# Performance work log

Measured on AMD Instinct MI355X. Metric: run time of the kernel, lower is better.

## Reference

```python
import jax, jax.numpy as jnp
import numpy as np

B, IN, H = 131072, 128, 128


def setup_inputs() -> dict:
    key = jax.random.key(0)
    ks = jax.random.split(key, 8)
    scale_W = 1.0 / np.sqrt(IN + H)
    scale_r = 1.0 / np.sqrt(H)
    return {
        "x": jax.random.normal(ks[0], (B, IN), jnp.float32),
        "h": jax.random.normal(ks[1], (B, H), jnp.float32),
        "c": jax.random.normal(ks[2], (B, H), jnp.float32),
        "n": jax.random.uniform(ks[3], (B, H), jnp.float32, 0.1, 1.0),
        "m": jax.random.normal(ks[4], (B, H), jnp.float32),
        "W": jax.random.normal(ks[5], (IN + H, 4 * H), jnp.float32) * scale_W,
        "r": jax.random.normal(ks[6], (H, 4 * H), jnp.float32) * scale_r,
        "b": jnp.zeros((4 * H,), jnp.float32),
    }


def reference(x, h, c, n, m, W, r, b):
    # fused gate pre-activations: [B, 4H]
    combined = jnp.concatenate((x, h), axis=1)
    gates = combined @ W + h @ r + b
    i_raw, f_raw, z_raw, o_raw = jnp.split(gates, 4, axis=1)
    i = jnp.exp(i_raw)
    f = jax.nn.sigmoid(f_raw)
    z = jnp.tanh(z_raw)
    o = jax.nn.sigmoid(o_raw)
    # log-domain stabilizer (max trick), faithful to source incl. m overwrite
    m_new = jnp.maximum(jnp.log(f) + m, jnp.log(i))
    i_prime = jnp.exp(jnp.log(i) - m_new)
    f_prime = jnp.exp(jnp.log(f) + m_new - m_new)  # == f, as in source
    c_new = f_prime * c + i_prime * z
    n_new = f_prime * n + i_prime
    h_tilde = c_new / n_new
    h_new = o * jnp.tanh(h_tilde)
    return (h_new, c_new, n_new, m_new)
```

## Files before the change

kernel.cpp:

```cpp
#include <hip/hip_runtime.h>
#include <cstdint>

#define NROWS 131072
#define HD    128
#define NDIM  512
#define OUTQ  16777216

using bf16x8 = __attribute__((ext_vector_type(8))) short;
using f32x4  = __attribute__((ext_vector_type(4))) float;

__device__ __forceinline__ uint32_t bf16rne(float f) {
  uint32_t u = __builtin_bit_cast(uint32_t, f);
  return (u + 0x7fffu + ((u >> 16) & 1u)) >> 16;
}

__device__ __forceinline__ float tanhf_fast(float v) {
  float a = __builtin_fabsf(v);
  float e = __expf(-2.0f * a);
  float t = (1.0f - e) * __builtin_amdgcn_rcpf(1.0f + e);
  return v < 0.0f ? -t : t;
}

__device__ __forceinline__ f32x4 ldv(const float* p) {
  return *reinterpret_cast<const f32x4*>(p);
}

#define ASYNC16(g, l)                                                        \
  __builtin_amdgcn_global_load_lds(                                          \
      (const __attribute__((address_space(1))) void*)(g),                    \
      (__attribute__((address_space(3))) void*)(l), 16, 0, 0)

__global__ __launch_bounds__(256) void pack_weights(
    const float* __restrict__ W, const float* __restrict__ r,
    uint16_t* __restrict__ Bp) {
  int idx = blockIdx.x * 256 + threadIdx.x;
  int l  = idx & 63;
  int ts = idx >> 6;
  int s  = ts & 7;
  int t  = ts >> 3;
  int g  = t >> 3;
  int u  = t & 7;
  int t2 = u >> 1;
  int p  = u & 1;
  int m  = l & 15;
  int ncol  = g * 128 + t2 * 32 + ((m >> 2) << 3) + p * 4 + (m & 3);
  int kbase = s * 32 + ((l >> 4) << 3);
  uint32_t w[4];
#pragma unroll
  for (int jj = 0; jj < 4; ++jj) {
    int k0 = kbase + 2 * jj;
    float v0 = W[k0 * NDIM + ncol];
    float v1 = W[(k0 + 1) * NDIM + ncol];
    if (k0 >= 128)     v0 += r[(k0 - 128) * NDIM + ncol];
    if (k0 + 1 >= 128) v1 += r[(k0 + 1 - 128) * NDIM + ncol];
    w[jj] = bf16rne(v0) | (bf16rne(v1) << 16);
  }
  reinterpret_cast<uint4*>(Bp)[idx] = make_uint4(w[0], w[1], w[2], w[3]);
}

__global__ __launch_bounds__(256, 3) void slstm_fused(
    const float* __restrict__ x,  const float* __restrict__ h,
    const float* __restrict__ cs, const float* __restrict__ ns,
    const float* __restrict__ ms, const float* __restrict__ bias,
    const uint16_t* __restrict__ Bp, float* __restrict__ out) {
  __shared__ __align__(16) char smem[32768];
  const int tid  = threadIdx.x;
  const int wave = tid >> 6;
  const int lane = tid & 63;
  const int row0 = blockIdx.x * 64;
  const int l15  = lane & 15;
  const int lg   = lane >> 4;

  const int    myrow = row0 + wave * 16 + l15;
  const size_t rbase = (size_t)myrow * HD;
  const int    jb8   = lg * 8;

  const char* wBytes = (const char*)Bp;
  {
    const char* gsrc = wBytes + (((size_t)(wave * 8 + 0) * 8) << 10) + (lane << 4);
    char* ldst = smem + (wave << 13);
#pragma unroll
    for (int k = 0; k < 8; ++k)
      ASYNC16(gsrc + (k << 10), ldst + (k << 10));
  }

  bf16x8 a[8];
#pragma unroll
  for (int s = 0; s < 8; ++s) {
    const float* src = (s < 4 ? x : h) + rbase + ((s & 3) * 32 + lg * 8);
    f32x4 v0 = ldv(src);
    f32x4 v1 = ldv(src + 4);
    bf16x8 pk;
    pk[0] = (short)bf16rne(v0[0]);
    pk[1] = (short)bf16rne(v0[1]);
    pk[2] = (short)bf16rne(v0[2]);
    pk[3] = (short)bf16rne(v0[3]);
    pk[4] = (short)bf16rne(v1[0]);
    pk[5] = (short)bf16rne(v1[1]);
    pk[6] = (short)bf16rne(v1[2]);
    pk[7] = (short)bf16rne(v1[3]);
    a[s] = pk;
  }

#pragma unroll
  for (int t2 = 0; t2 < 4; ++t2) {
    const int cb = t2 * 32 + jb8;

    __syncthreads();

    const f32x4 cvLo = ldv(cs + rbase + cb), cvHi = ldv(cs + rbase + cb + 4);
    const f32x4 nvLo = ldv(ns + rbase + cb), nvHi = ldv(ns + rbase + cb + 4);
    const f32x4 mvLo = ldv(ms + rbase + cb), mvHi = ldv(ms + rbase + cb + 4);

    f32x4 accI0 = {0,0,0,0}, accF0 = {0,0,0,0}, accZ0 = {0,0,0,0}, accO0 = {0,0,0,0};
#pragma unroll
    for (int s = 0; s < 8; ++s) {
      const int lo = lane << 4;
      bf16x8 wI = *reinterpret_cast<const bf16x8*>(smem + ((0 * 8 + s) << 10) + lo);
      bf16x8 wF = *reinterpret_cast<const bf16x8*>(smem + ((1 * 8 + s) << 10) + lo);
      bf16x8 wZ = *reinterpret_cast<const bf16x8*>(smem + ((2 * 8 + s) << 10) + lo);
      bf16x8 wO = *reinterpret_cast<const bf16x8*>(smem + ((3 * 8 + s) << 10) + lo);
      accI0 = __builtin_amdgcn_mfma_f32_16x16x32_bf16(wI, a[s], accI0, 0, 0, 0);
      accF0 = __builtin_amdgcn_mfma_f32_16x16x32_bf16(wF, a[s], accF0, 0, 0, 0);
      accZ0 = __builtin_amdgcn_mfma_f32_16x16x32_bf16(wZ, a[s], accZ0, 0, 0, 0);
      accO0 = __builtin_amdgcn_mfma_f32_16x16x32_bf16(wO, a[s], accO0, 0, 0, 0);
    }
    __syncthreads();

    {
      const char* gsrc = wBytes + (((size_t)(wave * 8 + (2 * t2 + 1)) * 8) << 10) + (lane << 4);
      char* ldst = smem + (wave << 13);
#pragma unroll
      for (int k = 0; k < 8; ++k)
        ASYNC16(gsrc + (k << 10), ldst + (k << 10));
    }
    __syncthreads();

    const f32x4 bIlo = ldv(bias + cb),        bIhi = ldv(bias + cb + 4);
    const f32x4 bFlo = ldv(bias + 128 + cb),  bFhi = ldv(bias + 128 + cb + 4);
    const f32x4 bZlo = ldv(bias + 256 + cb),  bZhi = ldv(bias + 256 + cb + 4);
    const f32x4 bOlo = ldv(bias + 384 + cb),  bOhi = ldv(bias + 384 + cb + 4);

    f32x4 accI1 = {0,0,0,0}, accF1 = {0,0,0,0}, accZ1 = {0,0,0,0}, accO1 = {0,0,0,0};
#pragma unroll
    for (int s = 0; s < 8; ++s) {
      const int lo = lane << 4;
      bf16x8 wI = *reinterpret_cast<const bf16x8*>(smem + ((0 * 8 + s) << 10) + lo);
      bf16x8 wF = *reinterpret_cast<const bf16x8*>(smem + ((1 * 8 + s) << 10) + lo);
      bf16x8 wZ = *reinterpret_cast<const bf16x8*>(smem + ((2 * 8 + s) << 10) + lo);
      bf16x8 wO = *reinterpret_cast<const bf16x8*>(smem + ((3 * 8 + s) << 10) + lo);
      accI1 = __builtin_amdgcn_mfma_f32_16x16x32_bf16(wI, a[s], accI1, 0, 0, 0);
      accF1 = __builtin_amdgcn_mfma_f32_16x16x32_bf16(wF, a[s], accF1, 0, 0, 0);
      accZ1 = __builtin_amdgcn_mfma_f32_16x16x32_bf16(wZ, a[s], accZ1, 0, 0, 0);
      accO1 = __builtin_amdgcn_mfma_f32_16x16x32_bf16(wO, a[s], accO1, 0, 0, 0);
    }
    __syncthreads();

    if (t2 < 3) {
      const char* gsrc = wBytes + (((size_t)(wave * 8 + (2 * t2 + 2)) * 8) << 10) + (lane << 4);
      char* ldst = smem + (wave << 13);
#pragma unroll
      for (int k = 0; k < 8; ++k)
        ASYNC16(gsrc + (k << 10), ldst + (k << 10));
    }

    f32x4 hnLo, hnHi, cnLo, cnHi, nnLo, nnHi, mnLo, mnHi;
#pragma unroll
    for (int d = 0; d < 8; ++d) {
      const int pp = d >> 2, rr = d & 3;
      const float i_raw = (pp ? accI1[rr] : accI0[rr]) + (pp ? bIhi[rr] : bIlo[rr]);
      const float f_raw = (pp ? accF1[rr] : accF0[rr]) + (pp ? bFhi[rr] : bFlo[rr]);
      const float z_raw = (pp ? accZ1[rr] : accZ0[rr]) + (pp ? bZhi[rr] : bZlo[rr]);
      const float o_raw = (pp ? accO1[rr] : accO0[rr]) + (pp ? bOhi[rr] : bOlo[rr]);
      const float cV = pp ? cvHi[rr] : cvLo[rr];
      const float nV = pp ? nvHi[rr] : nvLo[rr];
      const float mV = pp ? mvHi[rr] : mvLo[rr];
      float ef  = __expf(-f_raw);
      float den = 1.0f + ef;
      float fg  = __builtin_amdgcn_rcpf(den);
      float lgf = -__logf(den);
      float mnv = fmaxf(lgf + mV, i_raw);
      float ip  = __expf(i_raw - mnv);
      float zt  = tanhf_fast(z_raw);
      float og  = __builtin_amdgcn_rcpf(1.0f + __expf(-o_raw));
      float cnv = fg * cV + ip * zt;
      float nnv = fg * nV + ip;
      float hnv = og * tanhf_fast(cnv * __builtin_amdgcn_rcpf(nnv));
      if (pp == 0) { hnLo[rr] = hnv; cnLo[rr] = cnv; nnLo[rr] = nnv; mnLo[rr] = mnv; }
      else         { hnHi[rr] = hnv; cnHi[rr] = cnv; nnHi[rr] = nnv; mnHi[rr] = mnv; }
    }
    const size_t pbase = rbase + cb;
    *reinterpret_cast<f32x4*>(out + pbase)                = hnLo;
    *reinterpret_cast<f32x4*>(out + pbase + 4)            = hnHi;
    *reinterpret_cast<f32x4*>(out + OUTQ + pbase)         = cnLo;
    *reinterpret_cast<f32x4*>(out + OUTQ + pbase + 4)     = cnHi;
    *reinterpret_cast<f32x4*>(out + 2 * OUTQ + pbase)     = nnLo;
    *reinterpret_cast<f32x4*>(out + 2 * OUTQ + pbase + 4) = nnHi;
    *reinterpret_cast<f32x4*>(out + 3 * OUTQ + pbase)     = mnLo;
    *reinterpret_cast<f32x4*>(out + 3 * OUTQ + pbase + 4) = mnHi;
  }
}

extern "C" void kernel_launch(void* const* d_in, const int* in_sizes, int n_in,
                              void* d_out, int out_size, void* d_ws, size_t ws_size,
                              hipStream_t stream) {
  const float* x = (const float*)d_in[0];
  const float* h = (const float*)d_in[1];
  const float* c = (const float*)d_in[2];
  const float* n = (const float*)d_in[3];
  const float* m = (const float*)d_in[4];
  const float* W = (const float*)d_in[5];
  const float* r = (const float*)d_in[6];
  const float* b = (const float*)d_in[7];
  uint16_t* Bp = (uint16_t*)d_ws;

  pack_weights<<<64, 256, 0, stream>>>(W, r, Bp);
  slstm_fused<<<NROWS / 64, 256, 0, stream>>>(x, h, c, n, m, b, Bp, (float*)d_out);
}
```

Baseline: 149.2 us.

## Read packed weights directly from global memory instead of staging through LDS

Removes the LDS staging buffer, the async global-to-LDS copies and all block barriers. Each wave now loads its MFMA weight fragments straight from the packed global buffer, relying on L1/L2 caching since every block reads the same 128 KB of weights. The launch-bounds occupancy hint rises from 3 to 4 blocks per CU. The trade-off is more global and cache traffic per MFMA and exposed load latency in place of the shared LDS reuse across waves.

```diff
diff --git a/kernel.cpp b/kernel.cpp
--- a/kernel.cpp
+++ b/kernel.cpp
@@ -24,11 +24,6 @@
 __device__ __forceinline__ f32x4 ldv(const float* p) {
   return *reinterpret_cast<const f32x4*>(p);
 }
-
-#define ASYNC16(g, l)                                                        \
-  __builtin_amdgcn_global_load_lds(                                          \
-      (const __attribute__((address_space(1))) void*)(g),                    \
-      (__attribute__((address_space(3))) void*)(l), 16, 0, 0)
 
 __global__ __launch_bounds__(256) void pack_weights(
     const float* __restrict__ W, const float* __restrict__ r,
@@ -58,12 +53,11 @@
   reinterpret_cast<uint4*>(Bp)[idx] = make_uint4(w[0], w[1], w[2], w[3]);
 }
 
-__global__ __launch_bounds__(256, 3) void slstm_fused(
+__global__ __launch_bounds__(256, 4) void slstm_fused(
     const float* __restrict__ x,  const float* __restrict__ h,
     const float* __restrict__ cs, const float* __restrict__ ns,
     const float* __restrict__ ms, const float* __restrict__ bias,
     const uint16_t* __restrict__ Bp, float* __restrict__ out) {
-  __shared__ __align__(16) char smem[32768];
   const int tid  = threadIdx.x;
   const int wave = tid >> 6;
   const int lane = tid & 63;
@@ -74,15 +68,6 @@
   const int    myrow = row0 + wave * 16 + l15;
   const size_t rbase = (size_t)myrow * HD;
   const int    jb8   = lg * 8;
-
-  const char* wBytes = (const char*)Bp;
-  {
-    const char* gsrc = wBytes + (((size_t)(wave * 8 + 0) * 8) << 10) + (lane << 4);
-    char* ldst = smem + (wave << 13);
-#pragma unroll
-    for (int k = 0; k < 8; ++k)
-      ASYNC16(gsrc + (k << 10), ldst + (k << 10));
-  }
 
   bf16x8 a[8];
 #pragma unroll
@@ -102,67 +87,38 @@
     a[s] = pk;
   }
 
+  const bf16x8* __restrict__ Bf = reinterpret_cast<const bf16x8*>(Bp);
+
 #pragma unroll
   for (int t2 = 0; t2 < 4; ++t2) {
     const int cb = t2 * 32 + jb8;
-
-    __syncthreads();
 
     const f32x4 cvLo = ldv(cs + rbase + cb), cvHi = ldv(cs + rbase + cb + 4);
     const f32x4 nvLo = ldv(ns + rbase + cb), nvHi = ldv(ns + rbase + cb + 4);
     const f32x4 mvLo = ldv(ms + rbase + cb), mvHi = ldv(ms + rbase + cb + 4);
 
+    const int u0 = 2 * t2, u1 = 2 * t2 + 1;
     f32x4 accI0 = {0,0,0,0}, accF0 = {0,0,0,0}, accZ0 = {0,0,0,0}, accO0 = {0,0,0,0};
 #pragma unroll
     for (int s = 0; s < 8; ++s) {
-      const int lo = lane << 4;
-      bf16x8 wI = *reinterpret_cast<const bf16x8*>(smem + ((0 * 8 + s) << 10) + lo);
-      bf16x8 wF = *reinterpret_cast<const bf16x8*>(smem + ((1 * 8 + s) << 10) + lo);
-      bf16x8 wZ = *reinterpret_cast<const bf16x8*>(smem + ((2 * 8 + s) << 10) + lo);
-      bf16x8 wO = *reinterpret_cast<const bf16x8*>(smem + ((3 * 8 + s) << 10) + lo);
-      accI0 = __builtin_amdgcn_mfma_f32_16x16x32_bf16(wI, a[s], accI0, 0, 0, 0);
-      accF0 = __builtin_amdgcn_mfma_f32_16x16x32_bf16(wF, a[s], accF0, 0, 0, 0);
-      accZ0 = __builtin_amdgcn_mfma_f32_16x16x32_bf16(wZ, a[s], accZ0, 0, 0, 0);
-      accO0 = __builtin_amdgcn_mfma_f32_16x16x32_bf16(wO, a[s], accO0, 0, 0, 0);
+      accI0 = __builtin_amdgcn_mfma_f32_16x16x32_bf16(Bf[(size_t)(((0 * 8 + u0) * 8) + s) * 64 + lane], a[s], accI0, 0, 0, 0);
+      accF0 = __builtin_amdgcn_mfma_f32_16x16x32_bf16(Bf[(size_t)(((1 * 8 + u0) * 8) + s) * 64 + lane], a[s], accF0, 0, 0, 0);
+      accZ0 = __builtin_amdgcn_mfma_f32_16x16x32_bf16(Bf[(size_t)(((2 * 8 + u0) * 8) + s) * 64 + lane], a[s], accZ0, 0, 0, 0);
+      accO0 = __builtin_amdgcn_mfma_f32_16x16x32_bf16(Bf[(size_t)(((3 * 8 + u0) * 8) + s) * 64 + lane], a[s], accO0, 0, 0, 0);
     }
-    __syncthreads();
-
-    {
-      const char* gsrc = wBytes + (((size_t)(wave * 8 + (2 * t2 + 1)) * 8) << 10) + (lane << 4);
-      char* ldst = smem + (wave << 13);
+    f32x4 accI1 = {0,0,0,0}, accF1 = {0,0,0,0}, accZ1 = {0,0,0,0}, accO1 = {0,0,0,0};
 #pragma unroll
-      for (int k = 0; k < 8; ++k)
-        ASYNC16(gsrc + (k << 10), ldst + (k << 10));
+    for (int s = 0; s < 8; ++s) {
+      accI1 = __builtin_amdgcn_mfma_f32_16x16x32_bf16(Bf[(size_t)(((0 * 8 + u1) * 8) + s) * 64 + lane], a[s], accI1, 0, 0, 0);
+      accF1 = __builtin_amdgcn_mfma_f32_16x16x32_bf16(Bf[(size_t)(((1 * 8 + u1) * 8) + s) * 64 + lane], a[s], accF1, 0, 0, 0);
+      accZ1 = __builtin_amdgcn_mfma_f32_16x16x32_bf16(Bf[(size_t)(((2 * 8 + u1) * 8) + s) * 64 + lane], a[s], accZ1, 0, 0, 0);
+      accO1 = __builtin_amdgcn_mfma_f32_16x16x32_bf16(Bf[(size_t)(((3 * 8 + u1) * 8) + s) * 64 + lane], a[s], accO1, 0, 0, 0);
     }
-    __syncthreads();
 
     const f32x4 bIlo = ldv(bias + cb),        bIhi = ldv(bias + cb + 4);
     const f32x4 bFlo = ldv(bias + 128 + cb),  bFhi = ldv(bias + 128 + cb + 4);
     const f32x4 bZlo = ldv(bias + 256 + cb),  bZhi = ldv(bias + 256 + cb + 4);
     const f32x4 bOlo = ldv(bias + 384 + cb),  bOhi = ldv(bias + 384 + cb + 4);
-
-    f32x4 accI1 = {0,0,0,0}, accF1 = {0,0,0,0}, accZ1 = {0,0,0,0}, accO1 = {0,0,0,0};
-#pragma unroll
-    for (int s = 0; s < 8; ++s) {
-      const int lo = lane << 4;
-      bf16x8 wI = *reinterpret_cast<const bf16x8*>(smem + ((0 * 8 + s) << 10) + lo);
-      bf16x8 wF = *reinterpret_cast<const bf16x8*>(smem + ((1 * 8 + s) << 10) + lo);
-      bf16x8 wZ = *reinterpret_cast<const bf16x8*>(smem + ((2 * 8 + s) << 10) + lo);
-      bf16x8 wO = *reinterpret_cast<const bf16x8*>(smem + ((3 * 8 + s) << 10) + lo);
-      accI1 = __builtin_amdgcn_mfma_f32_16x16x32_bf16(wI, a[s], accI1, 0, 0, 0);
-      accF1 = __builtin_amdgcn_mfma_f32_16x16x32_bf16(wF, a[s], accF1, 0, 0, 0);
-      accZ1 = __builtin_amdgcn_mfma_f32_16x16x32_bf16(wZ, a[s], accZ1, 0, 0, 0);
-      accO1 = __builtin_amdgcn_mfma_f32_16x16x32_bf16(wO, a[s], accO1, 0, 0, 0);
-    }
-    __syncthreads();
-
-    if (t2 < 3) {
-      const char* gsrc = wBytes + (((size_t)(wave * 8 + (2 * t2 + 2)) * 8) << 10) + (lane << 4);
-      char* ldst = smem + (wave << 13);
-#pragma unroll
-      for (int k = 0; k < 8; ++k)
-        ASYNC16(gsrc + (k << 10), ldst + (k << 10));
-    }
 
     f32x4 hnLo, hnHi, cnLo, cnHi, nnLo, nnHi, mnLo, mnHi;
 #pragma unroll
```

New measurement: 309.0 us. +107.1%, slower.
